# Optimization experiments

Hardware: AMD Instinct MI355X
Metric: run time of the kernel (lower is better)

Reference implementation:

```python
import jax, jax.numpy as jnp
import numpy as np

B, N, E, H = 4, 512, 512, 8   # batch, tokens, embedding_channels (=KV_size_S), num_heads
C = 4 * E                      # KV_size_C
D = E // H                     # head dim
EPS = 1e-5                     # InstanceNorm2d default eps


def _inorm(x, axes):
    # InstanceNorm2d (affine=False): normalize over spatial axes with biased variance
    m = jnp.mean(x, axis=axes, keepdims=True)
    v = jnp.var(x, axis=axes, keepdims=True)
    return (x - m) * jax.lax.rsqrt(v + EPS)


def setup_inputs() -> dict:
    key = jax.random.key(0)
    ks = jax.random.split(key, 24)
    s = 0.02
    inp = {
        'emb1': jax.random.normal(ks[0], (B, N, E), jnp.float32),
        'emb2': jax.random.normal(ks[1], (B, N, E), jnp.float32),
        'emb3': jax.random.normal(ks[2], (B, N, E), jnp.float32),
        'emb4': jax.random.normal(ks[3], (B, N, E), jnp.float32),
        'emb_C': jax.random.normal(ks[4], (B, N, C), jnp.float32),
        'Wq1': jax.random.normal(ks[5], (E, E), jnp.float32) * s,
        'Wq2': jax.random.normal(ks[6], (E, E), jnp.float32) * s,
        'Wq3': jax.random.normal(ks[7], (E, E), jnp.float32) * s,
        'Wq4': jax.random.normal(ks[8], (E, E), jnp.float32) * s,
        'Wk': jax.random.normal(ks[9], (E, E), jnp.float32) * s,
        'Wv': jax.random.normal(ks[10], (E, E), jnp.float32) * s,
        'WqC': jax.random.normal(ks[11], (C, C), jnp.float32) * s,
        'WkC': jax.random.normal(ks[12], (C, C), jnp.float32) * s,
        'WvC': jax.random.normal(ks[13], (C, C), jnp.float32) * s,
        'Wo1': jax.random.normal(ks[14], (E, E), jnp.float32) * s,
        'Wo2': jax.random.normal(ks[15], (E, E), jnp.float32) * s,
        'Wo3': jax.random.normal(ks[16], (E, E), jnp.float32) * s,
        'Wo4': jax.random.normal(ks[17], (E, E), jnp.float32) * s,
    }
    return inp


def _heads(x):
    # [B, N, E] -> [B, H, N, D]
    b, n, _ = x.shape
    return x.reshape(b, n, H, D).transpose(0, 2, 1, 3)


def reference(emb1, emb2, emb3, emb4, emb_C,
              Wq1, Wq2, Wq3, Wq4, Wk, Wv, WqC, WkC, WvC,
              Wo1, Wo2, Wo3, Wo4):
    # ---- channel cross-attention ----
    QC = emb_C @ WqC.T            # [B, N, C]
    KC = emb_C @ WkC.T
    VC = emb_C @ WvC.T
    attn_c = jnp.einsum('bnc,bnd->bcd', QC, KC)        # [B, C, C]
    sim_c = jax.nn.softmax(_inorm(attn_c, (1, 2)), axis=-1)  # psi1 + softmax(dim=3)
    ctx_c = jnp.einsum('bcd,bnd->bcn', sim_c, VC)      # [B, C, N]
    T_hat = ctx_c.transpose(0, 2, 1)                   # [B, N, C]
    # split last dim into 4 chunks of E, concat along tokens -> [B, 4N, E]
    KV_S = jnp.concatenate(jnp.split(T_hat, 4, axis=2), axis=1)

    # ---- spatial multi-head cross-attention, shared K/V ----
    K = _heads(KV_S @ Wk.T)       # [B, H, 4N, D]
    V = _heads(KV_S @ Wv.T)

    outs = []
    for emb, Wq, Wo in ((emb1, Wq1, Wo1), (emb2, Wq2, Wo2),
                        (emb3, Wq3, Wo3), (emb4, Wq4, Wo4)):
        Q = _heads(emb @ Wq.T)                          # [B, H, N, D]
        attn = jnp.einsum('bhnd,bhmd->bhnm', Q, K)      # [B, H, N, 4N]
        sim = jax.nn.softmax(_inorm(attn, (2, 3)), axis=-1)  # psi2 + softmax
        ctx = jnp.einsum('bhnm,bhmd->bhnd', sim, V)     # [B, H, N, D]
        ctx = ctx.transpose(0, 2, 1, 3).reshape(emb.shape[0], emb.shape[1], E)
        outs.append(ctx @ Wo.T)
    return tuple(outs)
```

## Files before the change

### kernel.cpp

```cpp
#include <hip/hip_runtime.h>
#include <hip/hip_bf16.h>
#include <hip/hip_fp16.h>

typedef long long i64;
typedef unsigned int u32;
typedef __attribute__((ext_vector_type(8))) short bf16x8;
typedef __attribute__((ext_vector_type(4))) float f32x4;

#define MFMA_BF16 __builtin_amdgcn_mfma_f32_16x16x32_bf16
#define VMCNT(n)  asm volatile("s_waitcnt vmcnt(" #n ")" ::: "memory")
#define LGKM0     asm volatile("s_waitcnt lgkmcnt(0)" ::: "memory")
#define SBAR      __builtin_amdgcn_s_barrier()
#define SCHED0    __builtin_amdgcn_sched_barrier(0)

__device__ __forceinline__ void glds16(const void* g, void* l){
    __builtin_amdgcn_global_load_lds((const __attribute__((address_space(1))) u32*)g,
                                     (__attribute__((address_space(3))) u32*)l, 16, 0, 0);
}
__device__ __forceinline__ void split1(float x, ushort& h, ushort& l){
    unsigned b = __float_as_uint(x);
    h = (ushort)(b >> 16);
    float hf = __uint_as_float(b & 0xFFFF0000u);
    float lf = x - hf;
    l = (ushort)(__float_as_uint(lf) >> 16);
}
__device__ __forceinline__ float bfpair(ushort h, ushort l){
    return __uint_as_float((u32)h << 16) + __uint_as_float((u32)l << 16);
}
__device__ __forceinline__ bf16x8 fragS(const ushort* P, int row, int g){
    return *(const bf16x8*)&P[row*64 + (((g) ^ (row & 7)) << 3)];
}

struct P4 { const void* p[4]; };
struct I4 { int v[4]; };

struct PSJobs { const float* s[13]; ushort* d[13]; int st[14]; };
__global__ __launch_bounds__(256) void presplit(PSJobs J){
    int bid = blockIdx.x, j = 0;
    while (bid >= J.st[j+1]) ++j;
    i64 base = (i64)(bid - J.st[j])*2048 + threadIdx.x*8;
    i64 loOff = (i64)(J.st[j+1] - J.st[j])*2048;
    const float* sp = J.s[j]; ushort* dp = J.d[j];
    float4 a = *(const float4*)&sp[base];
    float4 b = *(const float4*)&sp[base+4];
    float v[8] = {a.x,a.y,a.z,a.w,b.x,b.y,b.z,b.w};
    ushort h[8], l[8];
    #pragma unroll
    for (int t = 0; t < 8; ++t) split1(v[t], h[t], l[t]);
    *(ushort4*)&dp[base]         = make_ushort4(h[0],h[1],h[2],h[3]);
    *(ushort4*)&dp[base+4]       = make_ushort4(h[4],h[5],h[6],h[7]);
    *(ushort4*)&dp[loOff+base]   = make_ushort4(l[0],l[1],l[2],l[3]);
    *(ushort4*)&dp[loOff+base+4] = make_ushort4(l[4],l[5],l[6],l[7]);
}

template<int TM, int OUT>
__global__ __launch_bounds__(256) void gemm_ps(
    P4 Ap, P4 Bp, P4 Cp, I4 cmode, float* __restrict__ stats,
    int K, int zdiv, int ci, int Y, int X,
    i64 ab2, i64 alda, i64 aLo,
    i64 bb2, i64 bldb, i64 bLo,
    i64 cb2, i64 cld, i64 cLo)
{
    constexpr int CW = (TM == 128) ? 64 : 32;
    constexpr int FJ = CW / 16;
    __shared__ ushort Ah[2][TM*32], Al[2][TM*32];
    __shared__ ushort Bh[2][4096], Bl[2][4096];
    __shared__ float sred[4], qred[4];
    const int q8 = gridDim.x >> 3;
    int wg = (blockIdx.x & 7) * q8 + (blockIdx.x >> 3);
    const int z2i = wg % ci; wg /= ci;
    const int y = wg % Y;    wg /= Y;
    const int x = wg % X;
    const int zo = wg / X;
    const int z = zo*ci + z2i;
    const int z1 = z / zdiv, z2 = z % zdiv;
    const int m0 = y*TM, n0 = x*128;

    const int tid = threadIdx.x, lane = tid & 63, wid = tid >> 6;
    const int wm = (TM == 128) ? (wid >> 1) : 0;
    const int wn = (TM == 128) ? (wid & 1) : wid;
    const int fr = lane & 15, kc = lane >> 4;
    const ushort* Aps = (const ushort*)Ap.p[z1] + (i64)z2*ab2 + (i64)m0*alda;
    const ushort* Bps = (const ushort*)Bp.p[z1] + (i64)z2*bb2 + (i64)n0*bldb;

    auto stageAB = [&](int k0, int pb){
        if constexpr (TM == 128) {
            #pragma unroll
            for (int q = 0; q < 2; ++q) {
                int r  = wid*32 + (lane >> 2) + q*16;
                int gs = (lane & 3) ^ ((r >> 1) & 3);
                const ushort* sa = Aps + (i64)r*alda + k0 + gs*8;
                glds16(sa,       &Ah[pb][(wid*32+q*16)*32]);
                glds16(sa + aLo, &Al[pb][(wid*32+q*16)*32]);
            }
        } else {
            int r  = wid*16 + (lane >> 2);
            int gs = (lane & 3) ^ ((r >> 1) & 3);
            const ushort* sa = Aps + (i64)r*alda + k0 + gs*8;
            glds16(sa,       &Ah[pb][(wid*16)*32]);
            glds16(sa + aLo, &Al[pb][(wid*16)*32]);
        }
        #pragma unroll
        for (int q = 0; q < 2; ++q) {
            int r  = wid*32 + (lane >> 2) + q*16;
            int gs = (lane & 3) ^ ((r >> 1) & 3);
            const ushort* sb = Bps + (i64)r*bldb + k0 + gs*8;
            glds16(sb,       &Bh[pb][(wid*32+q*16)*32]);
            glds16(sb + bLo, &Bl[pb][(wid*32+q*16)*32]);
        }
    };
    auto rd = [&](const ushort* P, int row, int kcc)->bf16x8 {
        return *(const bf16x8*)&P[row*32 + ((kcc ^ ((row >> 1) & 3)) << 3)];
    };

    f32x4 acc[4][FJ];
    #pragma unroll
    for (int i = 0; i < 4; ++i)
        #pragma unroll
        for (int j = 0; j < FJ; ++j) acc[i][j] = (f32x4){0.f,0.f,0.f,0.f};

    const int NT = K >> 5;
    stageAB(0, 0); stageAB(32, 1);

    for (int t = 0; t < NT; ++t) {
        const int cur = t & 1;
        if (t + 1 < NT) {
            if constexpr (TM == 128) { VMCNT(8); } else { VMCNT(6); }
        } else { VMCNT(0); }
        SBAR;
        bf16x8 a_h[4], a_l[4], b_h[FJ], b_l[FJ];
        #pragma unroll
        for (int i = 0; i < 4; ++i) {
            int row = wm*64 + i*16 + fr;
            a_h[i] = rd(Ah[cur], row, kc);
            a_l[i] = rd(Al[cur], row, kc);
        }
        #pragma unroll
        for (int j = 0; j < FJ; ++j) {
            int row = wn*CW + j*16 + fr;
            b_h[j] = rd(Bh[cur], row, kc);
            b_l[j] = rd(Bl[cur], row, kc);
        }
        __builtin_amdgcn_s_setprio(1);
        #pragma unroll
        for (int i = 0; i < 4; ++i)
            #pragma unroll
            for (int j = 0; j < FJ; ++j) {
                acc[i][j] = MFMA_BF16(a_h[i], b_h[j], acc[i][j], 0, 0, 0);
                acc[i][j] = MFMA_BF16(a_h[i], b_l[j], acc[i][j], 0, 0, 0);
                acc[i][j] = MFMA_BF16(a_l[i], b_h[j], acc[i][j], 0, 0, 0);
            }
        __builtin_amdgcn_s_setprio(0);
        LGKM0;
        SBAR;
        SCHED0;
        if (t + 2 < NT) stageAB((t+2) << 5, cur);
    }

    const i64 cbase = (i64)z2*cb2;
    if (OUT == 0) {
        float* C = (float*)Cp.p[z1];
        #pragma unroll
        for (int i = 0; i < 4; ++i)
            #pragma unroll
            for (int j = 0; j < FJ; ++j)
                #pragma unroll
                for (int r = 0; r < 4; ++r) {
                    int m = m0 + wm*64 + i*16 + kc*4 + r;
                    int n = n0 + wn*CW + j*16 + fr;
                    C[cbase + (i64)m*cld + n] = acc[i][j][r];
                }
    } else if (OUT == 1) {
        ushort* C = (ushort*)Cp.p[z1];
        const int cfg = cmode.v[z1];
        const int tr = cfg >> 30;
        const i64 ldv = cfg & 0x3FFFFFFF;
        #pragma unroll
        for (int i = 0; i < 4; ++i)
            #pragma unroll
            for (int j = 0; j < FJ; ++j)
                #pragma unroll
                for (int r = 0; r < 4; ++r) {
                    int m = m0 + wm*64 + i*16 + kc*4 + r;
                    int n = n0 + wn*CW + j*16 + fr;
                    ushort h, l; split1(acc[i][j][r], h, l);
                    i64 off = cbase + (tr ? (i64)n*ldv + m : (i64)m*ldv + n);
                    C[off] = h; C[off + cLo] = l;
                }
    } else if (OUT == 2) {
        __half* C = (__half*)Cp.p[z1];
        float ls = 0.f, lq = 0.f;
        #pragma unroll
        for (int i = 0; i < 4; ++i)
            #pragma unroll
            for (int j = 0; j < FJ; ++j)
                #pragma unroll
                for (int r = 0; r < 4; ++r) {
                    int m = m0 + wm*64 + i*16 + kc*4 + r;
                    int n = n0 + wn*CW + j*16 + fr;
                    float v = acc[i][j][r];
                    ls += v; lq += v*v;
                    C[cbase + (i64)m*cld + n] = __float2half(v);
                }
        #pragma unroll
        for (int off = 32; off; off >>= 1) { ls += __shfl_xor(ls, off); lq += __shfl_xor(lq, off); }
        if (lane == 0) { sred[wid] = ls; qred[wid] = lq; }
        __syncthreads();
        if (tid == 0) {
            atomicAdd(&stats[2*z],   sred[0]+sred[1]+sred[2]+sred[3]);
            atomicAdd(&stats[2*z+1], qred[0]+qred[1]+qred[2]+qred[3]);
        }
    } else {
        ushort* C = (ushort*)Cp.p[z1];
        #pragma unroll
        for (int i = 0; i < 4; ++i)
            #pragma unroll
            for (int j = 0; j < FJ; ++j)
                #pragma unroll
                for (int r = 0; r < 4; ++r) {
                    int m = m0 + wm*64 + i*16 + kc*4 + r;
                    int n = n0 + wn*CW + j*16 + fr;
                    ushort h, l; split1(acc[i][j][r], h, l);
                    i64 off = cbase + ((i64)(m >> 9) << 18) + ((i64)n << 9) + (m & 511);
                    C[off] = h; C[off + cLo] = l;
                }
    }
}

__global__ __launch_bounds__(256) void softmax_rows(
    __half* __restrict__ attn, ushort* __restrict__ lo,
    const float* __restrict__ stats, int rows_per_stat, float inv_count)
{
    const int ROWLEN = 2048;
    const int row = blockIdx.x;
    const int sidx = row / rows_per_stat;
    float sm = stats[2*sidx], sq = stats[2*sidx+1];
    float mean = sm * inv_count;
    float var = fmaxf(sq * inv_count - mean*mean, 0.f);
    float scale = rsqrtf(var + 1e-5f);
    __half* rp = attn + (i64)row * ROWLEN;
    ushort* hp = (ushort*)rp;
    ushort* lp = lo + (i64)row * ROWLEN;
    const int tid = threadIdx.x;
    float v[8]; float mx = -3.4e38f;
    #pragma unroll
    for (int s = 0; s < 8; ++s) { float x = __half2float(rp[tid + s*256]) * scale; v[s] = x; mx = fmaxf(mx, x); }
    #pragma unroll
    for (int off = 32; off; off >>= 1) mx = fmaxf(mx, __shfl_xor(mx, off));
    __shared__ float red[4];
    if ((tid & 63) == 0) red[tid >> 6] = mx;
    __syncthreads();
    mx = fmaxf(fmaxf(red[0], red[1]), fmaxf(red[2], red[3]));
    float ls = 0.f;
    #pragma unroll
    for (int s = 0; s < 8; ++s) { float e = __expf(v[s] - mx); v[s] = e; ls += e; }
    #pragma unroll
    for (int off = 32; off; off >>= 1) ls += __shfl_xor(ls, off);
    __syncthreads();
    if ((tid & 63) == 0) red[tid >> 6] = ls;
    __syncthreads();
    float inv = 1.f / (red[0] + red[1] + red[2] + red[3]);
    #pragma unroll
    for (int s = 0; s < 8; ++s) {
        ushort h, l; split1(v[s] * inv, h, l);
        hp[tid + s*256] = h; lp[tid + s*256] = l;
    }
}

__global__ __launch_bounds__(256) void gram64(
    const ushort* __restrict__ hi, i64 loOff, float* __restrict__ parts,
    i64 bstride, i64 zs2)
{
    __shared__ float T[16][68];
    __shared__ float csred[4][64];
    const int z = blockIdx.x;
    const int tid = threadIdx.x;
    const ushort* base = hi + (i64)(z>>3)*bstride + (i64)blockIdx.z*zs2
                       + (i64)blockIdx.y*256*512 + (z&7)*64;
    float g[4][4] = {{0.f}};
    float cs = 0.f;
    const int sr = tid >> 4, sc = (tid & 15) * 4;
    const int col = tid & 63, qq = tid >> 6;
    for (int grp = 0; grp < 16; ++grp) {
        i64 idx = (i64)(grp*16 + sr)*512 + sc;
        ushort4 hv = *(const ushort4*)&base[idx];
        ushort4 lv = *(const ushort4*)&base[loOff + idx];
        float4 ld;
        ld.x = bfpair(hv.x, lv.x); ld.y = bfpair(hv.y, lv.y);
        ld.z = bfpair(hv.z, lv.z); ld.w = bfpair(hv.w, lv.w);
        __syncthreads();
        *(float4*)&T[sr][sc] = ld;
        __syncthreads();
        #pragma unroll
        for (int rr = 0; rr < 16; ++rr) {
            const float4 a = *(const float4*)&T[rr][sr*4];
            const float4 b = *(const float4*)&T[rr][sc];
            g[0][0]+=a.x*b.x; g[0][1]+=a.x*b.y; g[0][2]+=a.x*b.z; g[0][3]+=a.x*b.w;
            g[1][0]+=a.y*b.x; g[1][1]+=a.y*b.y; g[1][2]+=a.y*b.z; g[1][3]+=a.y*b.w;
            g[2][0]+=a.z*b.x; g[2][1]+=a.z*b.y; g[2][2]+=a.z*b.z; g[2][3]+=a.z*b.w;
            g[3][0]+=a.w*b.x; g[3][1]+=a.w*b.y; g[3][2]+=a.w*b.z; g[3][3]+=a.w*b.w;
        }
        cs += T[qq*4+0][col] + T[qq*4+1][col] + T[qq*4+2][col] + T[qq*4+3][col];
    }
    float* outp = parts + (i64)((blockIdx.z*gridDim.y + blockIdx.y)*gridDim.x + blockIdx.x)*4160;
    #pragma unroll
    for (int xx = 0; xx < 4; ++xx)
        #pragma unroll
        for (int yy = 0; yy < 4; ++yy)
            outp[(sr*4+xx)*64 + sc + yy] = g[xx][yy];
    csred[qq][col] = cs;
    __syncthreads();
    if (tid < 64) outp[4096 + tid] = csred[0][tid]+csred[1][tid]+csred[2][tid]+csred[3][tid];
}

__global__ __launch_bounds__(256) void fin_stats(
    const float* __restrict__ gq, const float* __restrict__ gk,
    float* __restrict__ ss)
{
    const int z = blockIdx.x, s = blockIdx.y;
    const int tid = threadIdx.x;
    const int lane = tid & 63, wid = tid >> 6;
    const float* q0 = gq + (i64)((s*2+0)*32 + z)*4160;
    const float* q1 = gq + (i64)((s*2+1)*32 + z)*4160;
    float p2 = 0.f;
    for (int i = tid; i < 4096; i += 256) {
        float a = q0[i] + q1[i];
        float b = 0.f;
        #pragma unroll
        for (int c = 0; c < 8; ++c) b += gk[(i64)(c*32 + z)*4160 + i];
        p2 += a*b;
    }
    float p1 = 0.f;
    if (tid < 64) {
        float a = q0[4096+tid] + q1[4096+tid];
        float b = 0.f;
        #pragma unroll
        for (int c = 0; c < 8; ++c) b += gk[(i64)(c*32 + z)*4160 + 4096 + tid];
        p1 = a*b;
    }
    #pragma unroll
    for (int off = 32; off; off >>= 1) { p2 += __shfl_xor(p2, off); p1 += __shfl_xor(p1, off); }
    __shared__ float r2[4], r1[4];
    if (lane == 0) { r2[wid] = p2; r1[wid] = p1; }
    __syncthreads();
    if (tid == 0) {
        float S2 = r2[0]+r2[1]+r2[2]+r2[3];
        float S1 = r1[0]+r1[1]+r1[2]+r1[3];
        const float inv = 1.f/1048576.f;
        float mu = S1*inv;
        float var = fmaxf(S2*inv - mu*mu, 0.f);
        float sc = rsqrtf(var + 1e-5f);
        ss[(s*32+z)*2] = sc;
        ss[(s*32+z)*2+1] = sc*mu;
    }
}

__global__ __launch_bounds__(256) void flash_ps(
    const ushort* __restrict__ Qp, const ushort* __restrict__ Kp,
    const ushort* __restrict__ Vtp, const float* __restrict__ ss,
    ushort* __restrict__ ctxp)
{
    __shared__ ushort QPh[4096], QPl[4096];
    __shared__ ushort Kh[2][4096], Kl[2][4096];
    __shared__ ushort Vh[2][4096], Vl[2][4096];
    const int q8 = gridDim.x >> 3;
    int wg = (blockIdx.x & 7) * q8 + (blockIdx.x >> 3);
    const int qt = wg & 7, zz = (wg >> 3) & 31, s = wg >> 8;
    const int b = zz >> 3, hD = (zz & 7) * 64;
    const float scale = ss[(s*32+zz)*2], shift = ss[(s*32+zz)*2+1];
    const ushort* Qb = Qp + (i64)s*2097152 + (i64)b*262144 + (i64)(qt*64)*512 + hD;
    const ushort* Kb = Kp + (i64)b*1048576 + hD;
    const ushort* Vb = Vtp + (i64)b*1048576 + (i64)hD*2048;
    const int tid = threadIdx.x, lane = tid & 63, wid = tid >> 6;
    const int wq = wid >> 1, wk = wid & 1, fr = lane & 15, kc = lane >> 4;

    auto stage64 = [&](const ushort* src, i64 ld, i64 lo, ushort* Lh, ushort* Ll){
        #pragma unroll
        for (int q = 0; q < 2; ++q) {
            int rb = wid*16 + q*8;
            int r = rb + (lane >> 3);
            int gs = (lane & 7) ^ (r & 7);
            const ushort* p = src + (i64)r*ld + gs*8;
            glds16(p,      &Lh[rb*64]);
            glds16(p + lo, &Ll[rb*64]);
        }
    };

    stage64(Qb, 512, 1048576, QPh, QPl);
    stage64(Kb, 512, 4194304, Kh[0], Kl[0]);
    stage64(Vb, 2048, 4194304, Vh[0], Vl[0]);
    VMCNT(8); SBAR;
    bf16x8 qh[2][2], ql[2][2];
    #pragma unroll
    for (int i = 0; i < 2; ++i)
        #pragma unroll
        for (int ks = 0; ks < 2; ++ks) {
            int row = wq*32 + i*16 + fr;
            qh[i][ks] = fragS(QPh, row, ks*4 + kc);
            ql[i][ks] = fragS(QPl, row, ks*4 + kc);
        }
    LGKM0; SBAR;
    SCHED0;
    stage64(Kb + (i64)64*512, 512, 4194304, Kh[1], Kl[1]);
    stage64(Vb + 64, 2048, 4194304, Vh[1], Vl[1]);

    f32x4 ctx[2][2];
    #pragma unroll
    for (int i = 0; i < 2; ++i)
        #pragma unroll
        for (int j = 0; j < 2; ++j) ctx[i][j] = (f32x4){0.f,0.f,0.f,0.f};
    float den_lr[2][4] = {{0.f}};

    for (int t = 0; t < 32; ++t) {
        const int cur = t & 1;
        if (t < 31) { VMCNT(8); } else { VMCNT(0); }
        SBAR;
        f32x4 sacc[2][2];
        #pragma unroll
        for (int i = 0; i < 2; ++i)
            #pragma unroll
            for (int j = 0; j < 2; ++j) sacc[i][j] = (f32x4){0.f,0.f,0.f,0.f};
        #pragma unroll
        for (int ks = 0; ks < 2; ++ks) {
            bf16x8 khf[2], klf[2];
            #pragma unroll
            for (int j = 0; j < 2; ++j) {
                int row = wk*32 + j*16 + fr;
                khf[j] = fragS(Kh[cur], row, ks*4 + kc);
                klf[j] = fragS(Kl[cur], row, ks*4 + kc);
            }
            __builtin_amdgcn_s_setprio(1);
            #pragma unroll
            for (int i = 0; i < 2; ++i)
                #pragma unroll
                for (int j = 0; j < 2; ++j) {
                    sacc[i][j] = MFMA_BF16(qh[i][ks], khf[j], sacc[i][j], 0, 0, 0);
                    sacc[i][j] = MFMA_BF16(qh[i][ks], klf[j], sacc[i][j], 0, 0, 0);
                    sacc[i][j] = MFMA_BF16(ql[i][ks], khf[j], sacc[i][j], 0, 0, 0);
                }
            __builtin_amdgcn_s_setprio(0);
        }
        #pragma unroll
        for (int i = 0; i < 2; ++i)
            #pragma unroll
            for (int j = 0; j < 2; ++j)
                #pragma unroll
                for (int r = 0; r < 4; ++r) {
                    float p = __expf(sacc[i][j][r]*scale - shift);
                    den_lr[i][r] += p;
                    ushort h, l; split1(p, h, l);
                    int row = wq*32 + i*16 + kc*4 + r;
                    int col = wk*32 + j*16 + fr;
                    int pos = row*64 + ((((col>>3) ^ (row&7)) << 3) | (col & 7));
                    QPh[pos] = h; QPl[pos] = l;
                }
        LGKM0; SBAR;
        SCHED0;
        if (t < 30) stage64(Kb + (i64)((t+2)*64)*512, 512, 4194304, Kh[cur], Kl[cur]);
        #pragma unroll
        for (int ks = 0; ks < 2; ++ks) {
            bf16x8 vhf[2], vlf[2], pah[2], pal[2];
            #pragma unroll
            for (int j = 0; j < 2; ++j) {
                int row = wk*32 + j*16 + fr;
                vhf[j] = fragS(Vh[cur], row, ks*4 + kc);
                vlf[j] = fragS(Vl[cur], row, ks*4 + kc);
            }
            #pragma unroll
            for (int i = 0; i < 2; ++i) {
                int row = wq*32 + i*16 + fr;
                pah[i] = fragS(QPh, row, ks*4 + kc);
                pal[i] = fragS(QPl, row, ks*4 + kc);
            }
            __builtin_amdgcn_s_setprio(1);
            #pragma unroll
            for (int i = 0; i < 2; ++i)
                #pragma unroll
                for (int j = 0; j < 2; ++j) {
                    ctx[i][j] = MFMA_BF16(pah[i], vhf[j], ctx[i][j], 0, 0, 0);
                    ctx[i][j] = MFMA_BF16(pah[i], vlf[j], ctx[i][j], 0, 0, 0);
                    ctx[i][j] = MFMA_BF16(pal[i], vhf[j], ctx[i][j], 0, 0, 0);
                }
            __builtin_amdgcn_s_setprio(0);
        }
        LGKM0; SBAR;
        SCHED0;
        if (t < 30) stage64(Vb + (t+2)*64, 2048, 4194304, Vh[cur], Vl[cur]);
    }

    float* denf = (float*)QPl;
    #pragma unroll
    for (int i = 0; i < 2; ++i)
        #pragma unroll
        for (int r = 0; r < 4; ++r) {
            float d = den_lr[i][r];
            d += __shfl_xor(d, 1); d += __shfl_xor(d, 2);
            d += __shfl_xor(d, 4); d += __shfl_xor(d, 8);
            if (fr == 0) denf[wk*64 + wq*32 + i*16 + kc*4 + r] = d;
        }
    __syncthreads();
    ushort* Cb = ctxp + (i64)s*2097152 + (i64)b*262144;
    #pragma unroll
    for (int i = 0; i < 2; ++i)
        #pragma unroll
        for (int j = 0; j < 2; ++j)
            #pragma unroll
            for (int r = 0; r < 4; ++r) {
                int row = wq*32 + i*16 + kc*4 + r;
                int col = wk*32 + j*16 + fr;
                float dv = denf[row] + denf[64 + row];
                ushort h, l; split1(ctx[i][j][r] / dv, h, l);
                i64 off = (i64)(qt*64 + row)*512 + hD + col;
                Cb[off] = h; Cb[off + 1048576] = l;
            }
}

static inline P4 p4x(const void* a, const void* b, const void* c, const void* d){
    P4 x; x.p[0]=a; x.p[1]=b; x.p[2]=c; x.p[3]=d; return x;
}
static inline P4 p4x(const void* a){ return p4x(a,a,a,a); }
static inline I4 i4x(int a, int b, int c, int d){ I4 x; x.v[0]=a; x.v[1]=b; x.v[2]=c; x.v[3]=d; return x; }
#define TRC(ld) ((1<<30)|(ld))

extern "C" void kernel_launch(void* const* d_in, const int* in_sizes, int n_in,
                              void* d_out, int out_size, void* d_ws, size_t ws_size,
                              hipStream_t stream)
{
    (void)in_sizes; (void)n_in; (void)out_size;
    const float* emb[4] = {(const float*)d_in[0], (const float*)d_in[1],
                           (const float*)d_in[2], (const float*)d_in[3]};
    const float* embC = (const float*)d_in[4];
    const float* Wq[4] = {(const float*)d_in[5], (const float*)d_in[6],
                          (const float*)d_in[7], (const float*)d_in[8]};
    const float* Wk  = (const float*)d_in[9];
    const float* Wv  = (const float*)d_in[10];
    const float* WqC = (const float*)d_in[11];
    const float* WkC = (const float*)d_in[12];
    const float* WvC = (const float*)d_in[13];
    const float* Wo[4] = {(const float*)d_in[14], (const float*)d_in[15],
                          (const float*)d_in[16], (const float*)d_in[17]};
    float* out = (float*)d_out;

    char* ws = (char*)d_ws;
    const size_t MB = 1024*1024;
    if (ws_size < 128*MB + 512) return;
    auto U = [&](size_t mb){ return (ushort*)(ws + mb*MB); };
    float* stats = (float*)(ws + 122*MB);
    float* ssbuf = (float*)(ws + 122*MB + 1024);
    float* GKp   = (float*)(ws + 48*MB);
    float* GQp   = (float*)(ws + 53*MB);
    __half* scores = (__half*)(ws + 16*MB);

    hipMemsetAsync(stats, 0, 512, stream);

    {
        PSJobs J;
        const float* srcs[13] = {embC, WqC, WkC, WvC, Wk, Wv,
                                 Wq[0],Wq[1],Wq[2],Wq[3], Wo[0],Wo[1],Wo[2]};
        ushort* dsts[13] = {U(0),U(16),U(32),U(48),U(64),U(65),
                            U(66),U(67),U(68),U(69), U(70),U(71),U(72)};
        int blks[13] = {2048,2048,2048,2048,128,128, 128,128,128,128, 128,128,128};
        int a = 0;
        for (int j = 0; j < 13; ++j) { J.s[j]=srcs[j]; J.d[j]=dsts[j]; J.st[j]=a; a+=blks[j]; }
        J.st[13] = a;
        presplit<<<dim3(a), 256, 0, stream>>>(J);
    }
    gemm_ps<64,1><<<dim3(1536), 256, 0, stream>>>(
        p4x(U(0)), p4x(U(16), U(32), U(48), U(48)), p4x(U(74), U(90), U(106), U(106)),
        i4x(TRC(512), TRC(512), 2048, 2048), nullptr,
        2048, 4, 4, 8, 16,
        1048576, 2048, 4194304,   0, 2048, 4194304,   1048576, 0, 4194304);
    {
        PSJobs J;
        const float* srcs[13] = {emb[0], emb[1], emb[2], emb[3], Wo[3],
                                 nullptr,nullptr,nullptr,nullptr,nullptr,nullptr,nullptr,nullptr};
        ushort* dsts[13] = {U(0), U(4), U(8), U(12), U(73),
                            nullptr,nullptr,nullptr,nullptr,nullptr,nullptr,nullptr,nullptr};
        int blks[5] = {512,512,512,512,128};
        int a = 0;
        for (int j = 0; j < 5; ++j) { J.s[j]=srcs[j]; J.d[j]=dsts[j]; J.st[j]=a; a+=blks[j]; }
        for (int j = 5; j < 14; ++j) J.st[j] = a;
        presplit<<<dim3(a), 256, 0, stream>>>(J);
    }
    gemm_ps<128,2><<<dim3(1024), 256, 0, stream>>>(
        p4x(U(74)), p4x(U(90)), p4x(scores), i4x(0,0,0,0), stats,
        512, 4, 1, 16, 16,
        1048576, 512, 4194304,   1048576, 512, 4194304,   4194304, 2048, 0);
    softmax_rows<<<dim3(4*2048), 256, 0, stream>>>(scores, U(74), stats, 2048, 1.f/4194304.f);
    gemm_ps<64,3><<<dim3(512), 256, 0, stream>>>(
        p4x(U(16)), p4x(U(106)), p4x(U(48)), i4x(0,0,0,0), nullptr,
        2048, 4, 1, 32, 4,
        4194304, 2048, 30408704,   1048576, 2048, 4194304,   1048576, 0, 4194304);
    gemm_ps<128,1><<<dim3(512), 256, 0, stream>>>(
        p4x(U(48)), p4x(U(64), U(65), U(65), U(65)), p4x(U(74), U(90), U(90), U(90)),
        i4x(512, TRC(2048), 0, 0), nullptr,
        512, 4, 4, 16, 4,
        1048576, 512, 4194304,   0, 512, 262144,   1048576, 0, 4194304);
    gemm_ps<64,1><<<dim3(512), 256, 0, stream>>>(
        p4x(U(0), U(4), U(8), U(12)), p4x(U(66), U(67), U(68), U(69)),
        p4x(U(106), U(110), U(114), U(118)),
        i4x(512,512,512,512), nullptr,
        512, 4, 4, 8, 4,
        262144, 512, 1048576,   0, 512, 262144,   262144, 0, 1048576);
    gram64<<<dim3(32, 8, 1), 256, 0, stream>>>(U(74), 4194304, GKp, 1048576, 0);
    gram64<<<dim3(32, 2, 4), 256, 0, stream>>>(U(106), 1048576, GQp, 262144, 2097152);
    fin_stats<<<dim3(32, 4), 256, 0, stream>>>(GQp, GKp, ssbuf);
    flash_ps<<<dim3(1024), 256, 0, stream>>>(U(106), U(74), U(90), ssbuf, U(16));
    gemm_ps<64,0><<<dim3(512), 256, 0, stream>>>(
        p4x(U(16), U(20), U(24), U(28)), p4x(U(70), U(71), U(72), U(73)),
        p4x(out, out + 1048576, out + 2097152, out + 3145728),
        i4x(0,0,0,0), nullptr,
        512, 4, 4, 8, 4,
        262144, 512, 1048576,   0, 512, 262144,   262144, 512, 1048576);
}
```

Measured before the change: 704.6 us.

## Add 256x256-tile 8-wave split-bf16 GEMM for QKV projection and channel scores

Adds a new gemm_8p kernel with 512 threads, 256x256 output tiles and 128 KB of double-buffered LDS holding the hi/lo bf16 split operands. It stages the next K-slice inside the MFMA loop and raises wave priority around the MFMA bursts. The kernel replaces the smaller-tile gemm_ps launches for the QKV projection and the channel-score GEMM, cutting operand reloads from global memory per output. In exchange there are far fewer workgroups (192 and 256 on a 256-CU part, so under one wave of blocks or exactly one), lower occupancy, and heavy register use for the 128 accumulators.

```diff
diff --git a/kernel.cpp b/kernel.cpp
--- a/kernel.cpp
+++ b/kernel.cpp
@@ -51,6 +51,139 @@
     *(ushort4*)&dp[base+4]       = make_ushort4(h[4],h[5],h[6],h[7]);
     *(ushort4*)&dp[loOff+base]   = make_ushort4(l[0],l[1],l[2],l[3]);
     *(ushort4*)&dp[loOff+base+4] = make_ushort4(l[4],l[5],l[6],l[7]);
+}
+
+template<int OUT>
+__global__ __launch_bounds__(512) void gemm_8p(
+    P4 Ap, P4 Bp, P4 Cp, I4 cmode, float* __restrict__ stats,
+    int K, int zdiv, int ci, int Y, int X,
+    i64 ab2, i64 alda, i64 aLo,
+    i64 bb2, i64 bldb, i64 bLo,
+    i64 cb2, i64 cld, i64 cLo)
+{
+    __shared__ ushort Ah[2][8192], Al[2][8192], Bh[2][8192], Bl[2][8192];
+    __shared__ float sred[8], qred[8];
+    const int q8 = gridDim.x >> 3;
+    int wg = (blockIdx.x & 7) * q8 + (blockIdx.x >> 3);
+    const int z2i = wg % ci; wg /= ci;
+    const int y = wg % Y;    wg /= Y;
+    const int x = wg % X;
+    const int zo = wg / X;
+    const int z = zo*ci + z2i;
+    const int z1 = z / zdiv, z2 = z % zdiv;
+    const int m0 = y*256, n0 = x*256;
+
+    const int tid = threadIdx.x, lane = tid & 63, wid = tid >> 6;
+    const int wm = wid >> 2, wn = wid & 3, fr = lane & 15, kc = lane >> 4;
+    const ushort* Aps = (const ushort*)Ap.p[z1] + (i64)z2*ab2 + (i64)m0*alda;
+    const ushort* Bps = (const ushort*)Bp.p[z1] + (i64)z2*bb2 + (i64)n0*bldb;
+
+    auto stage4 = [&](int k0, int pb, int half){
+        int r  = half*128 + (tid >> 2);
+        int rb = half*128 + (wid << 4);
+        int gs = (tid & 3) ^ ((r >> 1) & 3);
+        const ushort* sa = Aps + (i64)r*alda + k0 + gs*8;
+        glds16(sa,       &Ah[pb][rb*32]);
+        glds16(sa + aLo, &Al[pb][rb*32]);
+        const ushort* sb = Bps + (i64)r*bldb + k0 + gs*8;
+        glds16(sb,       &Bh[pb][rb*32]);
+        glds16(sb + bLo, &Bl[pb][rb*32]);
+    };
+    auto rd = [&](const ushort* P, int row, int kcc)->bf16x8 {
+        return *(const bf16x8*)&P[row*32 + ((kcc ^ ((row >> 1) & 3)) << 3)];
+    };
+
+    f32x4 acc[8][4];
+    #pragma unroll
+    for (int i = 0; i < 8; ++i)
+        #pragma unroll
+        for (int j = 0; j < 4; ++j) acc[i][j] = (f32x4){0.f,0.f,0.f,0.f};
+
+    const int NT = K >> 5;
+    stage4(0, 0, 0); stage4(0, 0, 1);
+
+    for (int t = 0; t < NT; ++t) {
+        const int cur = t & 1;
+        VMCNT(0); SBAR;
+        bf16x8 b_h[4], b_l[4];
+        #pragma unroll
+        for (int p = 0; p < 4; ++p) {
+            bf16x8 a_h[2], a_l[2];
+            if (p == 0) {
+                #pragma unroll
+                for (int j = 0; j < 4; ++j) {
+                    int row = wn*64 + j*16 + fr;
+                    b_h[j] = rd(Bh[cur], row, kc);
+                    b_l[j] = rd(Bl[cur], row, kc);
+                }
+            }
+            #pragma unroll
+            for (int e = 0; e < 2; ++e) {
+                int row = wm*128 + (p*2 + e)*16 + fr;
+                a_h[e] = rd(Ah[cur], row, kc);
+                a_l[e] = rd(Al[cur], row, kc);
+            }
+            if (p < 2 && t + 1 < NT) stage4((t+1) << 5, cur ^ 1, p);
+            SBAR;
+            __builtin_amdgcn_s_setprio(1);
+            #pragma unroll
+            for (int e = 0; e < 2; ++e)
+                #pragma unroll
+                for (int j = 0; j < 4; ++j) {
+                    acc[p*2+e][j] = MFMA_BF16(a_h[e], b_h[j], acc[p*2+e][j], 0, 0, 0);
+                    acc[p*2+e][j] = MFMA_BF16(a_h[e], b_l[j], acc[p*2+e][j], 0, 0, 0);
+                    acc[p*2+e][j] = MFMA_BF16(a_l[e], b_h[j], acc[p*2+e][j], 0, 0, 0);
+                }
+            __builtin_amdgcn_s_setprio(0);
+            SBAR;
+        }
+    }
+
+    const i64 cbase = (i64)z2*cb2;
+    if (OUT == 1) {
+        ushort* C = (ushort*)Cp.p[z1];
+        const int cfg = cmode.v[z1];
+        const int tr = cfg >> 30;
+        const i64 ldv = cfg & 0x3FFFFFFF;
+        #pragma unroll
+        for (int i = 0; i < 8; ++i)
+            #pragma unroll
+            for (int j = 0; j < 4; ++j)
+                #pragma unroll
+                for (int r = 0; r < 4; ++r) {
+                    int m = m0 + wm*128 + i*16 + kc*4 + r;
+                    int n = n0 + wn*64 + j*16 + fr;
+                    ushort h, l; split1(acc[i][j][r], h, l);
+                    i64 off = cbase + (tr ? (i64)n*ldv + m : (i64)m*ldv + n);
+                    C[off] = h; C[off + cLo] = l;
+                }
+    } else {
+        __half* C = (__half*)Cp.p[z1];
+        float ls = 0.f, lq = 0.f;
+        #pragma unroll
+        for (int i = 0; i < 8; ++i)
+            #pragma unroll
+            for (int j = 0; j < 4; ++j)
+                #pragma unroll
+                for (int r = 0; r < 4; ++r) {
+                    int m = m0 + wm*128 + i*16 + kc*4 + r;
+                    int n = n0 + wn*64 + j*16 + fr;
+                    float v = acc[i][j][r];
+                    ls += v; lq += v*v;
+                    C[cbase + (i64)m*cld + n] = __float2half(v);
+                }
+        #pragma unroll
+        for (int off = 32; off; off >>= 1) { ls += __shfl_xor(ls, off); lq += __shfl_xor(lq, off); }
+        if (lane == 0) { sred[wid] = ls; qred[wid] = lq; }
+        __syncthreads();
+        if (tid == 0) {
+            float s = 0.f, qq = 0.f;
+            #pragma unroll
+            for (int w = 0; w < 8; ++w) { s += sred[w]; qq += qred[w]; }
+            atomicAdd(&stats[2*z],   s);
+            atomicAdd(&stats[2*z+1], qq);
+        }
+    }
 }
 
 template<int TM, int OUT>
@@ -565,10 +698,10 @@
         J.st[13] = a;
         presplit<<<dim3(a), 256, 0, stream>>>(J);
     }
-    gemm_ps<64,1><<<dim3(1536), 256, 0, stream>>>(
+    gemm_8p<1><<<dim3(192), 512, 0, stream>>>(
         p4x(U(0)), p4x(U(16), U(32), U(48), U(48)), p4x(U(74), U(90), U(106), U(106)),
         i4x(TRC(512), TRC(512), 2048, 2048), nullptr,
-        2048, 4, 4, 8, 16,
+        2048, 4, 4, 2, 8,
         1048576, 2048, 4194304,   0, 2048, 4194304,   1048576, 0, 4194304);
     {
         PSJobs J;
@@ -582,9 +715,9 @@
         for (int j = 5; j < 14; ++j) J.st[j] = a;
         presplit<<<dim3(a), 256, 0, stream>>>(J);
     }
-    gemm_ps<128,2><<<dim3(1024), 256, 0, stream>>>(
+    gemm_8p<2><<<dim3(256), 512, 0, stream>>>(
         p4x(U(74)), p4x(U(90)), p4x(scores), i4x(0,0,0,0), stats,
-        512, 4, 1, 16, 16,
+        512, 4, 1, 8, 8,
         1048576, 512, 4194304,   1048576, 512, 4194304,   4194304, 2048, 0);
     softmax_rows<<<dim3(4*2048), 256, 0, stream>>>(scores, U(74), stats, 2048, 1.f/4194304.f);
     gemm_ps<64,3><<<dim3(512), 256, 0, stream>>>(
```

After: 659.8 us. -6.4%, faster.
